# Performance work log

Measured on AMD Instinct MI355X. Metric: run time of the kernel, lower is better.

Reference implementation:

```python
import math
import jax, jax.numpy as jnp
import numpy as np

B, S = 4, 2048
D_MODEL, D_STATE = 1024, 256
KSIZE, CHUNK, STEPS = 5, 16, 2
TOPK, LOOKBACK = 8, 64


def setup_inputs() -> dict:
    key = jax.random.key(0)
    ks = jax.random.split(key, 12)
    gn = lambda k, shape, s: jax.random.normal(k, shape, jnp.float32) * s
    s_in = 1.0 / math.sqrt(D_MODEL)
    s_st = 1.0 / math.sqrt(D_STATE)
    inp = {}
    inp['x'] = gn(ks[0], (B, S, D_MODEL), 1.0)
    inp['Wi'] = gn(ks[1], (D_MODEL, D_STATE), s_in); inp['bi'] = jnp.zeros((D_STATE,), jnp.float32)
    inp['conv_w'] = gn(ks[2], (KSIZE, D_STATE), 1.0 / math.sqrt(KSIZE)); inp['conv_b'] = jnp.zeros((D_STATE,), jnp.float32)
    inp['Wp'] = gn(ks[3], (D_STATE, D_STATE), s_st); inp['bp'] = jnp.zeros((D_STATE,), jnp.float32)
    inp['Wh'] = gn(ks[4], (D_STATE, 3), s_st); inp['bh'] = jnp.zeros((3,), jnp.float32)
    inp['Wq'] = gn(ks[5], (D_STATE, D_STATE), s_st); inp['bq'] = jnp.zeros((D_STATE,), jnp.float32)
    inp['Wk'] = gn(ks[6], (D_STATE, D_STATE), s_st); inp['bk'] = jnp.zeros((D_STATE,), jnp.float32)
    inp['Wv'] = gn(ks[7], (D_STATE, D_STATE), s_st); inp['bv'] = jnp.zeros((D_STATE,), jnp.float32)
    inp['W1'] = gn(ks[8], (4 * D_STATE, D_STATE), 1.0 / math.sqrt(4 * D_STATE)); inp['b1'] = jnp.zeros((D_STATE,), jnp.float32)
    inp['W2'] = gn(ks[9], (D_STATE, D_STATE), s_st); inp['b2'] = jnp.zeros((D_STATE,), jnp.float32)
    # original zero-inits out_proj; use small random so outputs/grads are nontrivial
    inp['Wo'] = gn(ks[10], (D_STATE, D_MODEL), 0.02 * s_st); inp['bo'] = jnp.zeros((D_MODEL,), jnp.float32)
    return inp


def _forward(x, Wi, bi, conv_w, conv_b, Wp, bp, Wh, bh, Wq, bq, Wk, bk, Wv, bv, W1, b1, W2, b2, Wo, bo):
    bsz, seq, _ = x.shape
    dim = Wi.shape[1]
    h = x @ Wi + bi  # [B,S,Dstate]
    # banded window indices: window for token t covers tokens [t-LOOKBACK, t)
    pos = jnp.arange(seq)[:, None] + jnp.arange(LOOKBACK)[None, :]  # index into LOOKBACK-left-padded seq
    valid = (pos - LOOKBACK) >= 0  # [S,L] actual token index = pos - LOOKBACK, always < t
    cidx = jnp.arange(seq)[:, None] + jnp.arange(KSIZE)[None, :]
    scale = 1.0 / math.sqrt(dim)
    for _ in range(STEPS):
        # causal depthwise conv (left pad K-1)
        hp = jnp.pad(h, ((0, 0), (KSIZE - 1, 0), (0, 0)))
        mixed = jnp.einsum('bskd,kd->bsd', hp[:, cidx, :], conv_w) + conv_b
        # phrase pool: chunk means, project, broadcast back to tokens
        ph = h.reshape(bsz, seq // CHUNK, CHUNK, dim).mean(axis=2)
        pb = jnp.repeat(ph @ Wp + bp, CHUNK, axis=1)
        # semantic causal windowed top-k attention
        q = h @ Wq + bq
        k = h @ Wk + bk
        v = h @ Wv + bv
        kp = jnp.pad(k, ((0, 0), (LOOKBACK, 0), (0, 0)))
        scores = jnp.einsum('bsd,bsld->bsl', q, kp[:, pos, :]) * scale  # [B,S,L]
        scores = jnp.where(valid[None], scores, -jnp.inf)
        ts, tr = jax.lax.top_k(scores, TOPK)  # [B,S,K]
        m = ts.max(axis=-1, keepdims=True)
        e = jnp.exp(ts - jnp.where(jnp.isfinite(m), m, 0.0))  # -inf slots -> 0 weight
        w = e / jnp.maximum(e.sum(axis=-1, keepdims=True), 1e-30)  # token 0: all zero
        tok = jnp.clip(jnp.arange(seq)[None, :, None] - LOOKBACK + tr, 0, seq - 1)  # [B,S,K]
        vg = jnp.take_along_axis(v, tok.reshape(bsz, seq * TOPK, 1), axis=1).reshape(bsz, seq, TOPK, dim)
        summ = jnp.einsum('bsk,bskd->bsd', w, vg)
        # update MLP with halt gate
        ui = jnp.concatenate([h, mixed, pb, summ], axis=-1)
        delta = jnp.tanh(ui @ W1 + b1) @ W2 + b2
        gate = jax.nn.sigmoid(h @ Wh + bh)[..., 2:3]  # halt_gate channel
        h = h + delta * gate
    return x + (h @ Wo + bo)


def reference(x, Wi, bi, conv_w, conv_b, Wp, bp, Wh, bh, Wq, bq, Wk, bk, Wv, bv, W1, b1, W2, b2, Wo, bo):
    return _forward(x, Wi, bi, conv_w, conv_b, Wp, bp, Wh, bh, Wq, bq, Wk, bk, Wv, bv, W1, b1, W2, b2, Wo, bo)
```

## Files before the change

kernel.cpp:

```cpp
#include <hip/hip_runtime.h>
#include <math.h>

#define B_    4
#define S_    2048
#define BS_   8192
#define DM_   1024
#define DS_   256
#define LB_   64
#define TOPK_ 8

typedef unsigned short u16;
typedef __bf16 bf16x8 __attribute__((ext_vector_type(8)));
typedef float  f32x4  __attribute__((ext_vector_type(4)));

static __device__ __forceinline__ u16 f2bf(float f) {
    union { float f; unsigned u; } a; a.f = f;
    unsigned u = a.u;
    unsigned r = u + 0x7FFFu + ((u >> 16) & 1u);
    return (u16)(r >> 16);
}
static __device__ __forceinline__ float bf2f(u16 v) {
    union { unsigned u; float f; } a; a.u = ((unsigned)v) << 16; return a.f;
}
static __device__ __forceinline__ unsigned pack2(float a, float b) {
    return (unsigned)f2bf(a) | ((unsigned)f2bf(b) << 16);
}

#define GLD16(g, l) __builtin_amdgcn_global_load_lds(                         \
    (const __attribute__((address_space(1))) void*)(g),                       \
    (__attribute__((address_space(3))) void*)(l), 16, 0, 0)

template<int MF, int EPI>
__device__ __forceinline__ void epilogue(
    f32x4 (&acc)[MF][2], int bm, int bn, int wm, int wn, int lr, int lc,
    const float* __restrict__ bias, void* __restrict__ Cv, int N,
    const void* __restrict__ extra0v, const float* __restrict__ extra1)
{
    #pragma unroll
    for (int i = 0; i < MF; ++i) {
        #pragma unroll
        for (int j = 0; j < 2; ++j) {
            int col = bn + wn * 32 + j * 16 + lr;
            #pragma unroll
            for (int r = 0; r < 4; ++r) {
                int row = bm + wm * (MF * 16) + i * 16 + lc * 4 + r;
                float val = acc[i][j][r] + bias[col];
                if constexpr (EPI == 2) {
                    const u16* e0 = (const u16*)extra0v;
                    val = bf2f(e0[(size_t)row * N + col]) + val * extra1[row];
                    ((u16*)Cv)[(size_t)row * N + col] = f2bf(val);
                } else if constexpr (EPI == 3) {
                    const u16* e0 = (const u16*)extra0v;
                    ((float*)Cv)[(size_t)row * N + col] = bf2f(e0[(size_t)row * N + col]) + val;
                } else {
                    ((u16*)Cv)[(size_t)row * N + col] = f2bf(val);
                }
            }
        }
    }
}

template<int EPI>
__device__ __forceinline__ void mm256_dev(
    unsigned char* smem, int id, int nb, int gx,
    const u16* __restrict__ A, const u16* __restrict__ Bt,
    const float* __restrict__ bias, void* __restrict__ Cv,
    int N, const void* __restrict__ extra0v, const float* __restrict__ extra1)
{
    unsigned char* smA = smem;
    unsigned char* smB = smem + 32768;

    const int per = nb >> 3;
    const int nid = (id & 7) * per + (id >> 3);
    const int bx  = nid % gx, by = nid / gx;

    const int lane = threadIdx.x & 63, wid = threadIdx.x >> 6;
    const int wm   = wid >> 1, wn = wid & 1;
    const int bm   = by * 64, bn = bx * 64;
    const int lr   = lane & 15, lc = lane >> 4;
    const int lrow2 = lane >> 5;
    const int g_lin = lane & 31;

    #pragma unroll
    for (int t = 0; t < 8; ++t) {
        int rbase = wid * 16 + t * 2;
        int row   = rbase + lrow2;
        int gg    = g_lin ^ (row & 15);
        GLD16(A + (size_t)(bm + row) * 256 + gg * 8,
              smA + (size_t)rbase * 512);
    }
    #pragma unroll
    for (int t = 0; t < 8; ++t) {
        int rbase = wid * 16 + t * 2;
        int row   = rbase + lrow2;
        int gg    = g_lin ^ (row & 15);
        GLD16(Bt + (size_t)(bn + row) * 256 + gg * 8,
              smB + (size_t)rbase * 512);
    }
    __syncthreads();

    f32x4 acc[2][2] = {};
    #pragma unroll
    for (int kg = 0; kg < 8; ++kg) {
        bf16x8 af[2], bfr[2];
        #pragma unroll
        for (int i = 0; i < 2; ++i) {
            int m = wm * 32 + i * 16 + lr;
            af[i] = *reinterpret_cast<const bf16x8*>(
                smA + m * 512 + (((kg * 4 + lc) ^ (m & 15)) * 16));
        }
        #pragma unroll
        for (int j = 0; j < 2; ++j) {
            int n = wn * 32 + j * 16 + lr;
            bfr[j] = *reinterpret_cast<const bf16x8*>(
                smB + n * 512 + (((kg * 4 + lc) ^ (n & 15)) * 16));
        }
        #pragma unroll
        for (int i = 0; i < 2; ++i)
            #pragma unroll
            for (int j = 0; j < 2; ++j)
                acc[i][j] = __builtin_amdgcn_mfma_f32_16x16x32_bf16(
                    af[i], bfr[j], acc[i][j], 0, 0, 0);
    }

    epilogue<2, EPI>(acc, bm, bn, wm, wn, lr, lc, bias, Cv, N, extra0v, extra1);
}

template<int EPI>
__global__ __launch_bounds__(256) void mm256_k(
    const u16* __restrict__ A, const u16* __restrict__ Bt,
    const float* __restrict__ bias, void* __restrict__ Cv,
    int N, int gx,
    const void* __restrict__ extra0v, const float* __restrict__ extra1)
{
    __shared__ __align__(16) unsigned char smem[65536];
    mm256_dev<EPI>(smem, blockIdx.x, gridDim.x, gx, A, Bt, bias, Cv, N,
                   extra0v, extra1);
}

template<int MF, int EPI>
__device__ __forceinline__ void mm_dev(
    unsigned char* smem, int id, int nb, int gx,
    const u16* __restrict__ A, const u16* __restrict__ Bt,
    const float* __restrict__ bias, void* __restrict__ Cv,
    int K, int N,
    const void* __restrict__ extra0v, const float* __restrict__ extra1)
{
    constexpr int BM  = MF * 32;
    constexpr int ABY = BM * 256;
    constexpr int BBY = 64 * 256;

    const int per = nb >> 3;
    const int nid = (id & 7) * per + (id >> 3);
    const int bx  = nid % gx, by = nid / gx;

    const int tid  = threadIdx.x;
    const int lane = tid & 63, wid = tid >> 6;
    const int wm   = wid >> 1, wn = wid & 1;
    const int bm   = by * BM, bn = bx * 64;
    const int lr   = lane & 15, lc = lane >> 4;
    const int l16  = lane >> 4, lg = lane & 15;

    auto stage = [&](int buf, int k0) {
        unsigned char* sA = smem + buf * (ABY + BBY);
        unsigned char* sB = sA + ABY;
        #pragma unroll
        for (int t = 0; t < BM / 16; ++t) {
            int row = wid * (BM / 4) + t * 4 + l16;
            int gg  = lg ^ (row & 15);
            GLD16(A + (size_t)(bm + row) * K + k0 + gg * 8,
                  sA + (size_t)(wid * (BM / 4) + t * 4) * 256);
        }
        #pragma unroll
        for (int t = 0; t < 4; ++t) {
            int row = wid * 16 + t * 4 + l16;
            int gg  = lg ^ (row & 15);
            GLD16(Bt + (size_t)(bn + row) * K + k0 + gg * 8,
                  sB + (size_t)(wid * 16 + t * 4) * 256);
        }
    };

    f32x4 acc[MF][2] = {};

    stage(0, 0);
    __syncthreads();

    const int nt = K >> 7;
    for (int t = 0; t < nt; ++t) {
        if (t + 1 < nt) stage((t + 1) & 1, (t + 1) << 7);

        unsigned char* sA = smem + (t & 1) * (ABY + BBY);
        unsigned char* sB = sA + ABY;
        #pragma unroll
        for (int kk = 0; kk < 4; ++kk) {
            bf16x8 af[MF], bfr[2];
            #pragma unroll
            for (int i = 0; i < MF; ++i) {
                int m = wm * (MF * 16) + i * 16 + lr;
                af[i] = *reinterpret_cast<const bf16x8*>(
                    sA + m * 256 + (((kk * 4 + lc) ^ (m & 15)) * 16));
            }
            #pragma unroll
            for (int j = 0; j < 2; ++j) {
                int n = wn * 32 + j * 16 + lr;
                bfr[j] = *reinterpret_cast<const bf16x8*>(
                    sB + n * 256 + (((kk * 4 + lc) ^ (n & 15)) * 16));
            }
            #pragma unroll
            for (int i = 0; i < MF; ++i)
                #pragma unroll
                for (int j = 0; j < 2; ++j)
                    acc[i][j] = __builtin_amdgcn_mfma_f32_16x16x32_bf16(
                        af[i], bfr[j], acc[i][j], 0, 0, 0);
        }
        __syncthreads();
    }

    epilogue<MF, EPI>(acc, bm, bn, wm, wn, lr, lc, bias, Cv, N, extra0v, extra1);
}

template<int MF, int EPI>
__global__ __launch_bounds__(256) void mm_k(
    const u16* __restrict__ A, const u16* __restrict__ Bt,
    const float* __restrict__ bias, void* __restrict__ Cv,
    int K, int N, int gx,
    const void* __restrict__ extra0v, const float* __restrict__ extra1)
{
    __shared__ __align__(16) unsigned char smem[2 * (MF * 32 * 256 + 64 * 256)];
    mm_dev<MF, EPI>(smem, blockIdx.x, gridDim.x, gx, A, Bt, bias, Cv, K, N,
                    extra0v, extra1);
}

__global__ __launch_bounds__(256) void mm_ui_k(
    const u16* __restrict__ h, const u16* __restrict__ mixed,
    const u16* __restrict__ php, const u16* __restrict__ summ,
    const u16* __restrict__ W1t, const float* __restrict__ b1,
    u16* __restrict__ t)
{
    __shared__ __align__(16) unsigned char smem[65536];

    const int nb  = gridDim.x;
    const int per = nb >> 3;
    const int id  = blockIdx.x;
    const int nid = (id & 7) * per + (id >> 3);
    const int bx  = nid & 3, by = nid >> 2;

    const int tid  = threadIdx.x;
    const int lane = tid & 63, wid = tid >> 6;
    const int wm   = wid >> 1, wn = wid & 1;
    const int bm   = by * 64, bn = bx * 64;
    const int lr   = lane & 15, lc = lane >> 4;
    const int l16  = lane >> 4, lg = lane & 15;

    auto stage = [&](int buf, int k0) {
        const int seg = k0 >> 8, kb = k0 & 255;
        const u16* Asrc = (seg == 0) ? h : (seg == 1) ? mixed : (seg == 2) ? php : summ;
        unsigned char* sA = smem + buf * 32768;
        unsigned char* sB = sA + 16384;
        #pragma unroll
        for (int tt = 0; tt < 4; ++tt) {
            int row = wid * 16 + tt * 4 + l16;
            int gg  = lg ^ (row & 15);
            int rs  = bm + row;
            if (seg == 2) rs >>= 4;
            GLD16(Asrc + (size_t)rs * DS_ + kb + gg * 8,
                  sA + (size_t)(wid * 16 + tt * 4) * 256);
        }
        #pragma unroll
        for (int tt = 0; tt < 4; ++tt) {
            int row = wid * 16 + tt * 4 + l16;
            int gg  = lg ^ (row & 15);
            GLD16(W1t + (size_t)(bn + row) * 1024 + k0 + gg * 8,
                  sB + (size_t)(wid * 16 + tt * 4) * 256);
        }
    };

    f32x4 acc[2][2] = {};

    stage(0, 0);
    __syncthreads();

    for (int t8 = 0; t8 < 8; ++t8) {
        if (t8 + 1 < 8) stage((t8 + 1) & 1, (t8 + 1) << 7);

        unsigned char* sA = smem + (t8 & 1) * 32768;
        unsigned char* sB = sA + 16384;
        #pragma unroll
        for (int kk = 0; kk < 4; ++kk) {
            bf16x8 af[2], bfr[2];
            #pragma unroll
            for (int i = 0; i < 2; ++i) {
                int m = wm * 32 + i * 16 + lr;
                af[i] = *reinterpret_cast<const bf16x8*>(
                    sA + m * 256 + (((kk * 4 + lc) ^ (m & 15)) * 16));
            }
            #pragma unroll
            for (int j = 0; j < 2; ++j) {
                int n = wn * 32 + j * 16 + lr;
                bfr[j] = *reinterpret_cast<const bf16x8*>(
                    sB + n * 256 + (((kk * 4 + lc) ^ (n & 15)) * 16));
            }
            #pragma unroll
            for (int i = 0; i < 2; ++i)
                #pragma unroll
                for (int j = 0; j < 2; ++j)
                    acc[i][j] = __builtin_amdgcn_mfma_f32_16x16x32_bf16(
                        af[i], bfr[j], acc[i][j], 0, 0, 0);
        }
        __syncthreads();
    }

    #pragma unroll
    for (int i = 0; i < 2; ++i) {
        #pragma unroll
        for (int j = 0; j < 2; ++j) {
            int col = bn + wn * 32 + j * 16 + lr;
            #pragma unroll
            for (int r = 0; r < 4; ++r) {
                int row = bm + wm * 32 + i * 16 + lc * 4 + r;
                t[(size_t)row * DS_ + col] = f2bf(tanhf(acc[i][j][r] + b1[col]));
            }
        }
    }
}

__device__ __forceinline__ void conv_dev(
    unsigned char* smem, int cid,
    const u16* __restrict__ h, const float* __restrict__ conv_w,
    const float* __restrict__ conv_b, const float* __restrict__ Wh,
    const float* __restrict__ bh, const u16* __restrict__ Wpt,
    const float* __restrict__ bp, u16* __restrict__ mixed,
    u16* __restrict__ php, float* __restrict__ gate)
{
    float* gpart = (float*)smem;
    float* cm    = (float*)(smem + 256);
    const int blk = (cid & 7) * 64 + (cid >> 3);
    const int d = threadIdx.x;
    const int b = blk >> 7;
    const int s0 = (blk & 127) * 16;
    const u16* hb = h + (size_t)b * S_ * DS_;
    u16* mb = mixed + (size_t)b * S_ * DS_;

    const float w0 = conv_w[0 * DS_ + d], w1 = conv_w[1 * DS_ + d],
                w2 = conv_w[2 * DS_ + d], w3 = conv_w[3 * DS_ + d],
                w4 = conv_w[4 * DS_ + d];
    const float cb = conv_b[d];
    const float whd = Wh[d * 3 + 2];

    float a0 = (s0 >= 4) ? bf2f(hb[(size_t)(s0 - 4) * DS_ + d]) : 0.f;
    float a1 = (s0 >= 3) ? bf2f(hb[(size_t)(s0 - 3) * DS_ + d]) : 0.f;
    float a2 = (s0 >= 2) ? bf2f(hb[(size_t)(s0 - 2) * DS_ + d]) : 0.f;
    float a3 = (s0 >= 1) ? bf2f(hb[(size_t)(s0 - 1) * DS_ + d]) : 0.f;

    float sum = 0.f;
    #pragma unroll
    for (int tt = 0; tt < 16; ++tt) {
        int s = s0 + tt;
        float cur = bf2f(hb[(size_t)s * DS_ + d]);
        mb[(size_t)s * DS_ + d] = f2bf(w0 * a0 + w1 * a1 + w2 * a2 + w3 * a3 + w4 * cur + cb);
        sum += cur;
        float g = cur * whd;
        #pragma unroll
        for (int off = 32; off; off >>= 1) g += __shfl_down(g, off);
        if ((d & 63) == 0) gpart[tt * 4 + (d >> 6)] = g;
        a0 = a1; a1 = a2; a2 = a3; a3 = cur;
    }
    cm[d] = sum * (1.f / 16.f);
    __syncthreads();
    if (d < 16) {
        float gg = gpart[d * 4 + 0] + gpart[d * 4 + 1] + gpart[d * 4 + 2] + gpart[d * 4 + 3];
        gate[(size_t)b * S_ + s0 + d] = 1.f / (1.f + expf(-(gg + bh[2])));
    }
    float accp = bp[d];
    const u16* wr = Wpt + (size_t)d * 256;
    #pragma unroll
    for (int k = 0; k < 256; k += 8) {
        bf16x8 w8 = *reinterpret_cast<const bf16x8*>(wr + k);
        accp += cm[k]     * (float)w8[0] + cm[k + 1] * (float)w8[1]
              + cm[k + 2] * (float)w8[2] + cm[k + 3] * (float)w8[3]
              + cm[k + 4] * (float)w8[4] + cm[k + 5] * (float)w8[5]
              + cm[k + 6] * (float)w8[6] + cm[k + 7] * (float)w8[7];
    }
    php[(size_t)blk * DS_ + d] = f2bf(accp);
}

__global__ __launch_bounds__(256) void step_a_k(
    const u16* __restrict__ h, const u16* __restrict__ Wqkvt,
    const float* __restrict__ bqkv, u16* __restrict__ qkv,
    const float* __restrict__ conv_w, const float* __restrict__ conv_b,
    const float* __restrict__ Wh, const float* __restrict__ bh,
    const u16* __restrict__ Wpt, const float* __restrict__ bp,
    u16* __restrict__ mixed, u16* __restrict__ php, float* __restrict__ gate)
{
    __shared__ __align__(16) unsigned char smem[65536];
    if (blockIdx.x < 1536) {
        mm256_dev<0>(smem, blockIdx.x, 1536, 12, h, Wqkvt, bqkv, qkv,
                     768, nullptr, nullptr);
    } else {
        conv_dev(smem, blockIdx.x - 1536, h, conv_w, conv_b, Wh, bh,
                 Wpt, bp, mixed, php, gate);
    }
}

__global__ __launch_bounds__(256) void scores_k(
    const u16* __restrict__ qkv, float* __restrict__ scores)
{
    __shared__ __align__(16) unsigned char smem[65536];
    unsigned char* smQ = smem;
    unsigned char* smK = smem + 16384;
    float* Sld = reinterpret_cast<float*>(smem);

    const int bid = blockIdx.x;
    const int blk = (bid & 7) * 32 + (bid >> 3);
    const int t0 = blk * 32;
    const int b  = t0 >> 11;
    const int s0 = t0 & (S_ - 1);
    const int tid = threadIdx.x;
    const int lane = tid & 63, wid = tid >> 6;
    const int lr = lane & 15, lc = lane >> 4;
    const int qt  = wid & 1;
    const int ktb = (wid >> 1) * 3;
    const int lrow2 = lane >> 5;
    const int g_lin = lane & 31;

    #pragma unroll
    for (int t = 0; t < 4; ++t) {
        int rbase = wid * 8 + t * 2;
        int row   = rbase + lrow2;
        int gg    = g_lin ^ (row & 15);
        GLD16(qkv + (size_t)(t0 + row) * 768 + gg * 8,
              smQ + (size_t)rbase * 512);
    }
    #pragma unroll
    for (int t = 0; t < 12; ++t) {
        int rbase = wid * 24 + t * 2;
        int row   = rbase + lrow2;
        int krow  = s0 - 64 + row; if (krow < 0) krow = 0;
        int gg    = g_lin ^ (row & 15);
        GLD16(qkv + ((size_t)(b * S_) + krow) * 768 + 256 + gg * 8,
              smK + (size_t)rbase * 512);
    }
    __syncthreads();

    f32x4 acc[3] = {};
    #pragma unroll
    for (int ks = 0; ks < 8; ++ks) {
        int m = qt * 16 + lr;
        bf16x8 af = *reinterpret_cast<const bf16x8*>(
            smQ + m * 512 + (((ks * 4 + lc) ^ (m & 15)) * 16));
        #pragma unroll
        for (int j = 0; j < 3; ++j) {
            int n = (ktb + j) * 16 + lr;
            bf16x8 bv = *reinterpret_cast<const bf16x8*>(
                smK + n * 512 + (((ks * 4 + lc) ^ (n & 15)) * 16));
            acc[j] = __builtin_amdgcn_mfma_f32_16x16x32_bf16(af, bv, acc[j], 0, 0, 0);
        }
    }
    __syncthreads();

    #pragma unroll
    for (int j = 0; j < 3; ++j) {
        int col = (ktb + j) * 16 + lr;
        #pragma unroll
        for (int r = 0; r < 4; ++r) {
            int row = qt * 16 + lc * 4 + r;
            Sld[row * 97 + col] = acc[j][r];
        }
    }
    __syncthreads();

    #pragma unroll
    for (int it = 0; it < 8; ++it) {
        int e = tid + it * 256;
        int i = e >> 6, l = e & 63;
        scores[(size_t)(t0 + i) * 64 + l] = Sld[i * 97 + i + l] * 0.0625f;
    }
}

__global__ __launch_bounds__(256) void select_k(
    const float* __restrict__ scores, const u16* __restrict__ qkv,
    u16* __restrict__ summ)
{
    const int bid = blockIdx.x;
    const int sb  = (bid & 7) * 256 + (bid >> 3);
    const int m   = sb * 4 + (threadIdx.x >> 6);
    const int b = m >> 11;
    const int s = m & (S_ - 1);
    const int lane = threadIdx.x & 63;

    float sc = (s - LB_ + lane >= 0) ? scores[(size_t)m * 64 + lane] : -INFINITY;

    float vals[TOPK_]; int idxs[TOPK_];
    #pragma unroll
    for (int t = 0; t < TOPK_; ++t) {
        float mv = sc; int mi = lane;
        #pragma unroll
        for (int off = 32; off; off >>= 1) {
            float ov = __shfl_xor(mv, off);
            int   oi = __shfl_xor(mi, off);
            if (ov > mv || (ov == mv && oi < mi)) { mv = ov; mi = oi; }
        }
        vals[t] = mv; idxs[t] = mi;
        if (lane == mi) sc = -INFINITY;
    }

    const float mref = (vals[0] == -INFINITY) ? 0.f : vals[0];
    float e[TOPK_], ssum = 0.f;
    #pragma unroll
    for (int t = 0; t < TOPK_; ++t) { e[t] = expf(vals[t] - mref); ssum += e[t]; }
    const float inv = 1.f / fmaxf(ssum, 1e-30f);

    float o0 = 0.f, o1 = 0.f, o2 = 0.f, o3 = 0.f;
    #pragma unroll
    for (int t = 0; t < TOPK_; ++t) {
        float wt = e[t] * inv;
        int tok = s - LB_ + idxs[t];
        tok = min(max(tok, 0), S_ - 1);
        ushort4 vv = *reinterpret_cast<const ushort4*>(
            qkv + ((size_t)(b * S_) + tok) * 768 + 512 + lane * 4);
        o0 += wt * bf2f(vv.x);
        o1 += wt * bf2f(vv.y);
        o2 += wt * bf2f(vv.z);
        o3 += wt * bf2f(vv.w);
    }
    ushort4 pk;
    pk.x = f2bf(o0); pk.y = f2bf(o1); pk.z = f2bf(o2); pk.w = f2bf(o3);
    *reinterpret_cast<ushort4*>(summ + (size_t)m * DS_ + lane * 4) = pk;
}

__global__ __launch_bounds__(256) void prep_all_k(
    const float* __restrict__ x,
    const float* __restrict__ Wi, const float* __restrict__ Wq,
    const float* __restrict__ Wk, const float* __restrict__ Wv,
    const float* __restrict__ Wp, const float* __restrict__ W1,
    const float* __restrict__ W2, const float* __restrict__ Wo,
    const float* __restrict__ bq, const float* __restrict__ bk,
    const float* __restrict__ bv,
    u16* __restrict__ xb,
    u16* __restrict__ Wit, u16* __restrict__ Wqkvt, u16* __restrict__ Wpt,
    u16* __restrict__ W1t, u16* __restrict__ W2t, u16* __restrict__ Wot,
    float* __restrict__ bqkv)
{
    const int bid0 = blockIdx.x;
    if (bid0 < 4096) {
        int i = (bid0 * 256 + threadIdx.x) * 8;
        float4 a = *reinterpret_cast<const float4*>(x + i);
        float4 b = *reinterpret_cast<const float4*>(x + i + 4);
        uint4 g;
        g.x = pack2(a.x, a.y); g.y = pack2(a.z, a.w);
        g.z = pack2(b.x, b.y); g.w = pack2(b.z, b.w);
        *reinterpret_cast<uint4*>(xb + i) = g;
        return;
    }
    const int bid = bid0 - 4096;
    if (bid >= 1088) {
        for (int i = threadIdx.x; i < 768; i += 256) {
            float v = (i < 256) ? bq[i] : (i < 512) ? bk[i - 256] : bv[i - 512];
            bqkv[i] = v;
        }
        return;
    }
    const float* in; u16* out; int K, N, t;
    if (bid < 256)      { in = Wi; out = Wit;             K = 1024; N = 256;  t = bid; }
    else if (bid < 320) { in = Wq; out = Wqkvt;           K = 256;  N = 256;  t = bid - 256; }
    else if (bid < 384) { in = Wk; out = Wqkvt + 256*256; K = 256;  N = 256;  t = bid - 320; }
    else if (bid < 448) { in = Wv; out = Wqkvt + 512*256; K = 256;  N = 256;  t = bid - 384; }
    else if (bid < 512) { in = Wp; out = Wpt;             K = 256;  N = 256;  t = bid - 448; }
    else if (bid < 768) { in = W1; out = W1t;             K = 1024; N = 256;  t = bid - 512; }
    else if (bid < 832) { in = W2; out = W2t;             K = 256;  N = 256;  t = bid - 768; }
    else                { in = Wo; out = Wot;             K = 256;  N = 1024; t = bid - 832; }
    const int tilesX = N >> 5;
    const int n0 = (t % tilesX) * 32, k0 = (t / tilesX) * 32;
    __shared__ float tl[32][33];
    const int cx = threadIdx.x & 31, cy = threadIdx.x >> 5;
    #pragma unroll
    for (int r = 0; r < 32; r += 8)
        tl[cy + r][cx] = in[(size_t)(k0 + cy + r) * N + n0 + cx];
    __syncthreads();
    #pragma unroll
    for (int r = 0; r < 32; r += 8)
        out[(size_t)(n0 + cy + r) * K + k0 + cx] = f2bf(tl[cx][cy + r]);
}

extern "C" void kernel_launch(void* const* d_in, const int* in_sizes, int n_in,
                              void* d_out, int out_size, void* d_ws, size_t ws_size,
                              hipStream_t stream)
{
    const float* x      = (const float*)d_in[0];
    const float* Wi     = (const float*)d_in[1];
    const float* bi     = (const float*)d_in[2];
    const float* conv_w = (const float*)d_in[3];
    const float* conv_b = (const float*)d_in[4];
    const float* Wp     = (const float*)d_in[5];
    const float* bp     = (const float*)d_in[6];
    const float* Wh     = (const float*)d_in[7];
    const float* bh     = (const float*)d_in[8];
    const float* Wq     = (const float*)d_in[9];
    const float* bq     = (const float*)d_in[10];
    const float* Wk     = (const float*)d_in[11];
    const float* bk     = (const float*)d_in[12];
    const float* Wv     = (const float*)d_in[13];
    const float* bv     = (const float*)d_in[14];
    const float* W1     = (const float*)d_in[15];
    const float* b1     = (const float*)d_in[16];
    const float* W2     = (const float*)d_in[17];
    const float* b2     = (const float*)d_in[18];
    const float* Wo     = (const float*)d_in[19];
    const float* bo     = (const float*)d_in[20];
    float* out = (float*)d_out;

    char* p = (char*)d_ws;
    auto alloc = [&](size_t bytes) { char* r = p; p += (bytes + 255) & ~(size_t)255; return r; };

    u16*  xb     = (u16*)alloc((size_t)BS_ * DM_ * 2);
    u16*  h      = (u16*)alloc((size_t)BS_ * DS_ * 2);
    u16*  mixed  = (u16*)alloc((size_t)BS_ * DS_ * 2);
    u16*  qkv    = (u16*)alloc((size_t)BS_ * 768 * 2);
    u16*  sm     = (u16*)alloc((size_t)BS_ * DS_ * 2);
    u16*  tb     = (u16*)alloc((size_t)BS_ * DS_ * 2);
    u16*  php    = (u16*)alloc((size_t)512 * DS_ * 2);
    float* gate  = (float*)alloc((size_t)BS_ * 4);
    float* scores= (float*)alloc((size_t)BS_ * 64 * 4);
    float* bqkv  = (float*)alloc(768 * 4);
    u16* Wit     = (u16*)alloc((size_t)256 * 1024 * 2);
    u16* Wqkvt   = (u16*)alloc((size_t)768 * 256 * 2);
    u16* Wpt     = (u16*)alloc((size_t)256 * 256 * 2);
    u16* W1t     = (u16*)alloc((size_t)256 * 1024 * 2);
    u16* W2t     = (u16*)alloc((size_t)256 * 256 * 2);
    u16* Wot     = (u16*)alloc((size_t)1024 * 256 * 2);

    dim3 blk(256);

    prep_all_k<<<5185, blk, 0, stream>>>(x, Wi, Wq, Wk, Wv, Wp, W1, W2, Wo,
                                         bq, bk, bv, xb,
                                         Wit, Wqkvt, Wpt, W1t, W2t, Wot, bqkv);

    mm_k<2, 0><<<512, blk, 0, stream>>>(xb, Wit, bi, h, DM_, DS_, 4, nullptr, nullptr);

    for (int step = 0; step < 2; ++step) {
        step_a_k<<<2048, blk, 0, stream>>>(h, Wqkvt, bqkv, qkv,
                                           conv_w, conv_b, Wh, bh, Wpt, bp,
                                           mixed, php, gate);
        scores_k<<<256, blk, 0, stream>>>(qkv, scores);
        select_k<<<2048, blk, 0, stream>>>(scores, qkv, sm);
        mm_ui_k<<<512, blk, 0, stream>>>(h, mixed, php, sm, W1t, b1, tb);
        mm256_k<2><<<512, blk, 0, stream>>>(tb, W2t, b2, h, DS_, 4, h, gate);
    }

    mm256_k<3><<<2048, blk, 0, stream>>>(h, Wot, bo, out, DM_, 16, xb, nullptr);
}
```

Baseline: 146.1 us.

## Use single-buffered 256-wide K slabs in GEMMs and bitonic-sort top-k selection

Replaces the double-buffered 128-wide K pipeline in the input projection and the W1 update GEMM with four sequential 256-wide K slabs loaded into one buffer, sharing a common slab MFMA helper. This halves the number of barriers and tile stages, but load and compute no longer overlap within a block. The top-k selection swaps eight serial wavefront max-reductions for one 64-lane bitonic sort followed by broadcasts of the top eight, which should cut shuffle work. Ties are still ordered by lower index, matching the previous rule.

```diff
diff --git a/kernel.cpp b/kernel.cpp
--- a/kernel.cpp
+++ b/kernel.cpp
@@ -60,6 +60,34 @@
     }
 }
 
+__device__ __forceinline__ void slab_mfma(
+    unsigned char* smA, unsigned char* smB, f32x4 (&acc)[2][2],
+    int wm, int wn, int lr, int lc)
+{
+    #pragma unroll
+    for (int kg = 0; kg < 8; ++kg) {
+        bf16x8 af[2], bfr[2];
+        #pragma unroll
+        for (int i = 0; i < 2; ++i) {
+            int m = wm * 32 + i * 16 + lr;
+            af[i] = *reinterpret_cast<const bf16x8*>(
+                smA + m * 512 + (((kg * 4 + lc) ^ (m & 15)) * 16));
+        }
+        #pragma unroll
+        for (int j = 0; j < 2; ++j) {
+            int n = wn * 32 + j * 16 + lr;
+            bfr[j] = *reinterpret_cast<const bf16x8*>(
+                smB + n * 512 + (((kg * 4 + lc) ^ (n & 15)) * 16));
+        }
+        #pragma unroll
+        for (int i = 0; i < 2; ++i)
+            #pragma unroll
+            for (int j = 0; j < 2; ++j)
+                acc[i][j] = __builtin_amdgcn_mfma_f32_16x16x32_bf16(
+                    af[i], bfr[j], acc[i][j], 0, 0, 0);
+    }
+}
+
 template<int EPI>
 __device__ __forceinline__ void mm256_dev(
     unsigned char* smem, int id, int nb, int gx,
@@ -86,42 +114,19 @@
         int rbase = wid * 16 + t * 2;
         int row   = rbase + lrow2;
         int gg    = g_lin ^ (row & 15);
-        GLD16(A + (size_t)(bm + row) * 256 + gg * 8,
-              smA + (size_t)rbase * 512);
+        GLD16(A + (size_t)(bm + row) * 256 + gg * 8, smA + (size_t)rbase * 512);
     }
     #pragma unroll
     for (int t = 0; t < 8; ++t) {
         int rbase = wid * 16 + t * 2;
         int row   = rbase + lrow2;
         int gg    = g_lin ^ (row & 15);
-        GLD16(Bt + (size_t)(bn + row) * 256 + gg * 8,
-              smB + (size_t)rbase * 512);
+        GLD16(Bt + (size_t)(bn + row) * 256 + gg * 8, smB + (size_t)rbase * 512);
     }
     __syncthreads();
 
     f32x4 acc[2][2] = {};
-    #pragma unroll
-    for (int kg = 0; kg < 8; ++kg) {
-        bf16x8 af[2], bfr[2];
-        #pragma unroll
-        for (int i = 0; i < 2; ++i) {
-            int m = wm * 32 + i * 16 + lr;
-            af[i] = *reinterpret_cast<const bf16x8*>(
-                smA + m * 512 + (((kg * 4 + lc) ^ (m & 15)) * 16));
-        }
-        #pragma unroll
-        for (int j = 0; j < 2; ++j) {
-            int n = wn * 32 + j * 16 + lr;
-            bfr[j] = *reinterpret_cast<const bf16x8*>(
-                smB + n * 512 + (((kg * 4 + lc) ^ (n & 15)) * 16));
-        }
-        #pragma unroll
-        for (int i = 0; i < 2; ++i)
-            #pragma unroll
-            for (int j = 0; j < 2; ++j)
-                acc[i][j] = __builtin_amdgcn_mfma_f32_16x16x32_bf16(
-                    af[i], bfr[j], acc[i][j], 0, 0, 0);
-    }
+    slab_mfma(smA, smB, acc, wm, wn, lr, lc);
 
     epilogue<2, EPI>(acc, bm, bn, wm, wn, lr, lc, bias, Cv, N, extra0v, extra1);
 }
@@ -138,97 +143,56 @@
                    extra0v, extra1);
 }
 
-template<int MF, int EPI>
-__device__ __forceinline__ void mm_dev(
-    unsigned char* smem, int id, int nb, int gx,
+template<int EPI>
+__global__ __launch_bounds__(256) void mm1024_k(
     const u16* __restrict__ A, const u16* __restrict__ Bt,
     const float* __restrict__ bias, void* __restrict__ Cv,
-    int K, int N,
+    int N, int gx,
     const void* __restrict__ extra0v, const float* __restrict__ extra1)
 {
-    constexpr int BM  = MF * 32;
-    constexpr int ABY = BM * 256;
-    constexpr int BBY = 64 * 256;
-
+    __shared__ __align__(16) unsigned char smem[65536];
+    unsigned char* smA = smem;
+    unsigned char* smB = smem + 32768;
+
+    const int nb  = gridDim.x;
     const int per = nb >> 3;
+    const int id  = blockIdx.x;
     const int nid = (id & 7) * per + (id >> 3);
     const int bx  = nid % gx, by = nid / gx;
 
-    const int tid  = threadIdx.x;
-    const int lane = tid & 63, wid = tid >> 6;
+    const int lane = threadIdx.x & 63, wid = threadIdx.x >> 6;
     const int wm   = wid >> 1, wn = wid & 1;
-    const int bm   = by * BM, bn = bx * 64;
+    const int bm   = by * 64, bn = bx * 64;
     const int lr   = lane & 15, lc = lane >> 4;
-    const int l16  = lane >> 4, lg = lane & 15;
-
-    auto stage = [&](int buf, int k0) {
-        unsigned char* sA = smem + buf * (ABY + BBY);
-        unsigned char* sB = sA + ABY;
-        #pragma unroll
-        for (int t = 0; t < BM / 16; ++t) {
-            int row = wid * (BM / 4) + t * 4 + l16;
-            int gg  = lg ^ (row & 15);
-            GLD16(A + (size_t)(bm + row) * K + k0 + gg * 8,
-                  sA + (size_t)(wid * (BM / 4) + t * 4) * 256);
-        }
-        #pragma unroll
-        for (int t = 0; t < 4; ++t) {
-            int row = wid * 16 + t * 4 + l16;
-            int gg  = lg ^ (row & 15);
-            GLD16(Bt + (size_t)(bn + row) * K + k0 + gg * 8,
-                  sB + (size_t)(wid * 16 + t * 4) * 256);
-        }
-    };
-
-    f32x4 acc[MF][2] = {};
-
-    stage(0, 0);
-    __syncthreads();
-
-    const int nt = K >> 7;
-    for (int t = 0; t < nt; ++t) {
-        if (t + 1 < nt) stage((t + 1) & 1, (t + 1) << 7);
-
-        unsigned char* sA = smem + (t & 1) * (ABY + BBY);
-        unsigned char* sB = sA + ABY;
-        #pragma unroll
-        for (int kk = 0; kk < 4; ++kk) {
-            bf16x8 af[MF], bfr[2];
-            #pragma unroll
-            for (int i = 0; i < MF; ++i) {
-                int m = wm * (MF * 16) + i * 16 + lr;
-                af[i] = *reinterpret_cast<const bf16x8*>(
-                    sA + m * 256 + (((kk * 4 + lc) ^ (m & 15)) * 16));
-            }
-            #pragma unroll
-            for (int j = 0; j < 2; ++j) {
-                int n = wn * 32 + j * 16 + lr;
-                bfr[j] = *reinterpret_cast<const bf16x8*>(
-                    sB + n * 256 + (((kk * 4 + lc) ^ (n & 15)) * 16));
-            }
-            #pragma unroll
-            for (int i = 0; i < MF; ++i)
-                #pragma unroll
-                for (int j = 0; j < 2; ++j)
-                    acc[i][j] = __builtin_amdgcn_mfma_f32_16x16x32_bf16(
-                        af[i], bfr[j], acc[i][j], 0, 0, 0);
+    const int lrow2 = lane >> 5;
+    const int g_lin = lane & 31;
+
+    f32x4 acc[2][2] = {};
+
+    #pragma unroll
+    for (int s = 0; s < 4; ++s) {
+        if (s) __syncthreads();
+        #pragma unroll
+        for (int t = 0; t < 8; ++t) {
+            int rbase = wid * 16 + t * 2;
+            int row   = rbase + lrow2;
+            int gg    = g_lin ^ (row & 15);
+            GLD16(A + (size_t)(bm + row) * 1024 + s * 256 + gg * 8,
+                  smA + (size_t)rbase * 512);
+        }
+        #pragma unroll
+        for (int t = 0; t < 8; ++t) {
+            int rbase = wid * 16 + t * 2;
+            int row   = rbase + lrow2;
+            int gg    = g_lin ^ (row & 15);
+            GLD16(Bt + (size_t)(bn + row) * 1024 + s * 256 + gg * 8,
+                  smB + (size_t)rbase * 512);
         }
         __syncthreads();
-    }
-
-    epilogue<MF, EPI>(acc, bm, bn, wm, wn, lr, lc, bias, Cv, N, extra0v, extra1);
-}
-
-template<int MF, int EPI>
-__global__ __launch_bounds__(256) void mm_k(
-    const u16* __restrict__ A, const u16* __restrict__ Bt,
-    const float* __restrict__ bias, void* __restrict__ Cv,
-    int K, int N, int gx,
-    const void* __restrict__ extra0v, const float* __restrict__ extra1)
-{
-    __shared__ __align__(16) unsigned char smem[2 * (MF * 32 * 256 + 64 * 256)];
-    mm_dev<MF, EPI>(smem, blockIdx.x, gridDim.x, gx, A, Bt, bias, Cv, K, N,
-                    extra0v, extra1);
+        slab_mfma(smA, smB, acc, wm, wn, lr, lc);
+    }
+
+    epilogue<2, EPI>(acc, bm, bn, wm, wn, lr, lc, bias, Cv, N, extra0v, extra1);
 }
 
 __global__ __launch_bounds__(256) void mm_ui_k(
@@ -238,6 +202,8 @@
     u16* __restrict__ t)
 {
     __shared__ __align__(16) unsigned char smem[65536];
+    unsigned char* smA = smem;
+    unsigned char* smB = smem + 32768;
 
     const int nb  = gridDim.x;
     const int per = nb >> 3;
@@ -245,69 +211,38 @@
     const int nid = (id & 7) * per + (id >> 3);
     const int bx  = nid & 3, by = nid >> 2;
 
-    const int tid  = threadIdx.x;
-    const int lane = tid & 63, wid = tid >> 6;
+    const int lane = threadIdx.x & 63, wid = threadIdx.x >> 6;
     const int wm   = wid >> 1, wn = wid & 1;
     const int bm   = by * 64, bn = bx * 64;
     const int lr   = lane & 15, lc = lane >> 4;
-    const int l16  = lane >> 4, lg = lane & 15;
-
-    auto stage = [&](int buf, int k0) {
-        const int seg = k0 >> 8, kb = k0 & 255;
-        const u16* Asrc = (seg == 0) ? h : (seg == 1) ? mixed : (seg == 2) ? php : summ;
-        unsigned char* sA = smem + buf * 32768;
-        unsigned char* sB = sA + 16384;
-        #pragma unroll
-        for (int tt = 0; tt < 4; ++tt) {
-            int row = wid * 16 + tt * 4 + l16;
-            int gg  = lg ^ (row & 15);
-            int rs  = bm + row;
-            if (seg == 2) rs >>= 4;
-            GLD16(Asrc + (size_t)rs * DS_ + kb + gg * 8,
-                  sA + (size_t)(wid * 16 + tt * 4) * 256);
-        }
-        #pragma unroll
-        for (int tt = 0; tt < 4; ++tt) {
-            int row = wid * 16 + tt * 4 + l16;
-            int gg  = lg ^ (row & 15);
-            GLD16(W1t + (size_t)(bn + row) * 1024 + k0 + gg * 8,
-                  sB + (size_t)(wid * 16 + tt * 4) * 256);
-        }
-    };
+    const int lrow2 = lane >> 5;
+    const int g_lin = lane & 31;
 
     f32x4 acc[2][2] = {};
 
-    stage(0, 0);
-    __syncthreads();
-
-    for (int t8 = 0; t8 < 8; ++t8) {
-        if (t8 + 1 < 8) stage((t8 + 1) & 1, (t8 + 1) << 7);
-
-        unsigned char* sA = smem + (t8 & 1) * 32768;
-        unsigned char* sB = sA + 16384;
-        #pragma unroll
-        for (int kk = 0; kk < 4; ++kk) {
-            bf16x8 af[2], bfr[2];
-            #pragma unroll
-            for (int i = 0; i < 2; ++i) {
-                int m = wm * 32 + i * 16 + lr;
-                af[i] = *reinterpret_cast<const bf16x8*>(
-                    sA + m * 256 + (((kk * 4 + lc) ^ (m & 15)) * 16));
-            }
-            #pragma unroll
-            for (int j = 0; j < 2; ++j) {
-                int n = wn * 32 + j * 16 + lr;
-                bfr[j] = *reinterpret_cast<const bf16x8*>(
-                    sB + n * 256 + (((kk * 4 + lc) ^ (n & 15)) * 16));
-            }
-            #pragma unroll
-            for (int i = 0; i < 2; ++i)
-                #pragma unroll
-                for (int j = 0; j < 2; ++j)
-                    acc[i][j] = __builtin_amdgcn_mfma_f32_16x16x32_bf16(
-                        af[i], bfr[j], acc[i][j], 0, 0, 0);
+    #pragma unroll
+    for (int s = 0; s < 4; ++s) {
+        const u16* Asrc = (s == 0) ? h : (s == 1) ? mixed : (s == 2) ? php : summ;
+        if (s) __syncthreads();
+        #pragma unroll
+        for (int tt = 0; tt < 8; ++tt) {
+            int rbase = wid * 16 + tt * 2;
+            int row   = rbase + lrow2;
+            int gg    = g_lin ^ (row & 15);
+            int rs    = bm + row;
+            if (s == 2) rs >>= 4;
+            GLD16(Asrc + (size_t)rs * 256 + gg * 8, smA + (size_t)rbase * 512);
+        }
+        #pragma unroll
+        for (int tt = 0; tt < 8; ++tt) {
+            int rbase = wid * 16 + tt * 2;
+            int row   = rbase + lrow2;
+            int gg    = g_lin ^ (row & 15);
+            GLD16(W1t + (size_t)(bn + row) * 1024 + s * 256 + gg * 8,
+                  smB + (size_t)rbase * 512);
         }
         __syncthreads();
+        slab_mfma(smA, smB, acc, wm, wn, lr, lc);
     }
 
     #pragma unroll
@@ -488,20 +423,28 @@
     const int s = m & (S_ - 1);
     const int lane = threadIdx.x & 63;
 
-    float sc = (s - LB_ + lane >= 0) ? scores[(size_t)m * 64 + lane] : -INFINITY;
+    float v = (s - LB_ + lane >= 0) ? scores[(size_t)m * 64 + lane] : -INFINITY;
+    int idx = lane;
+
+    #pragma unroll
+    for (int k = 2; k <= 64; k <<= 1) {
+        #pragma unroll
+        for (int j = k >> 1; j > 0; j >>= 1) {
+            float ov = __shfl_xor(v, j);
+            int   oi = __shfl_xor(idx, j);
+            bool mineFirst = (v > ov) || (v == ov && idx < oi);
+            bool lowLane  = (lane & j) == 0;
+            bool dirFirst = (lane & k) == 0;
+            bool keep = (lowLane == dirFirst) ? mineFirst : !mineFirst;
+            if (!keep) { v = ov; idx = oi; }
+        }
+    }
 
     float vals[TOPK_]; int idxs[TOPK_];
     #pragma unroll
     for (int t = 0; t < TOPK_; ++t) {
-        float mv = sc; int mi = lane;
-        #pragma unroll
-        for (int off = 32; off; off >>= 1) {
-            float ov = __shfl_xor(mv, off);
-            int   oi = __shfl_xor(mi, off);
-            if (ov > mv || (ov == mv && oi < mi)) { mv = ov; mi = oi; }
-        }
-        vals[t] = mv; idxs[t] = mi;
-        if (lane == mi) sc = -INFINITY;
+        vals[t] = __shfl(v, t);
+        idxs[t] = __shfl(idx, t);
     }
 
     const float mref = (vals[0] == -INFINITY) ? 0.f : vals[0];
@@ -635,7 +578,7 @@
                                          bq, bk, bv, xb,
                                          Wit, Wqkvt, Wpt, W1t, W2t, Wot, bqkv);
 
-    mm_k<2, 0><<<512, blk, 0, stream>>>(xb, Wit, bi, h, DM_, DS_, 4, nullptr, nullptr);
+    mm1024_k<0><<<512, blk, 0, stream>>>(xb, Wit, bi, h, DS_, 4, nullptr, nullptr);
 
     for (int step = 0; step < 2; ++step) {
         step_a_k<<<2048, blk, 0, stream>>>(h, Wqkvt, bqkv, qkv,
```

Measured after the change: 138.0 us (median of 2 runs). 5.6% less time.
